# Performance work log

Hardware: AMD Instinct MI355X
Metric: run time of the kernel (lower is better)

The kernel has to match this reference:

```python
import jax, jax.numpy as jnp
import numpy as np

B, N, H = 4, 256, 512
P = 128  # game_physics_params


def _init(key, shape, scale=0.02):
    return jax.random.normal(key, shape, dtype=jnp.float32) * scale


def setup_inputs() -> dict:
    key = jax.random.key(0)
    ks = jax.random.split(key, 16)
    return {
        "object_features": jax.random.normal(ks[0], (B, N, H), dtype=jnp.float32),
        # physics_predictor: H -> 512 -> P
        "pp_w1": _init(ks[1], (H, 512)), "pp_b1": jnp.zeros((512,), jnp.float32),
        "pp_w2": _init(ks[2], (512, P)), "pp_b2": jnp.zeros((P,), jnp.float32),
        # collision_detector: 2H -> 256 -> 128 -> 1
        "cd_w1": _init(ks[3], (2 * H, 256)), "cd_b1": jnp.zeros((256,), jnp.float32),
        "cd_w2": _init(ks[4], (256, 128)), "cd_b2": jnp.zeros((128,), jnp.float32),
        "cd_w3": _init(ks[5], (128, 1)), "cd_b3": jnp.zeros((1,), jnp.float32),
        # velocity / force heads: H -> 3
        "vel_w": _init(ks[6], (H, 3)), "vel_b": jnp.zeros((3,), jnp.float32),
        "frc_w": _init(ks[7], (H, 3)), "frc_b": jnp.zeros((3,), jnp.float32),
    }


def reference(object_features, pp_w1, pp_b1, pp_w2, pp_b2,
              cd_w1, cd_b1, cd_w2, cd_b2, cd_w3, cd_b3,
              vel_w, vel_b, frc_w, frc_b):
    x = object_features  # [B, N, H]
    # physics predictor MLP
    p = jax.nn.relu(x @ pp_w1 + pp_b1) @ pp_w2 + pp_b2  # [B, N, P]
    mass = jax.nn.sigmoid(p[..., 0:1]) * 100.0
    friction = jax.nn.sigmoid(p[..., 1:2])
    elasticity = jax.nn.sigmoid(p[..., 2:3])
    density = jax.nn.sigmoid(p[..., 3:4]) * 10.0
    velocities = x @ vel_w + vel_b  # [B, N, 3]
    forces = x @ frc_w + frc_b      # [B, N, 3]

    # vectorized pairwise collision detection over upper-triangle pairs
    iu, ju = np.triu_indices(N, k=1)  # static index arrays, length Np = N(N-1)/2
    pairs = jnp.concatenate([x[:, iu], x[:, ju]], axis=-1)  # [B, Np, 2H]
    h = jax.nn.relu(pairs @ cd_w1 + cd_b1)
    h = jax.nn.relu(h @ cd_w2 + cd_b2)
    prob = jax.nn.sigmoid(h @ cd_w3 + cd_b3)[..., 0]  # [B, Np]
    collision_matrix = jnp.zeros((x.shape[0], N, N), dtype=x.dtype)
    collision_matrix = collision_matrix.at[:, iu, ju].set(prob).at[:, ju, iu].set(prob)

    return (mass, friction, elasticity, density, velocities, forces, collision_matrix)
```

## Files before the change

kernel.cpp:

```cpp
#include <hip/hip_runtime.h>
#include <hip/hip_bf16.h>

typedef __attribute__((ext_vector_type(8))) short bf16x8;
typedef __attribute__((ext_vector_type(4))) float f32x4;

__device__ __forceinline__ float sigmoidf_(float v) {
    return 1.0f / (1.0f + __expf(-v));
}
__device__ __forceinline__ short f2bf(float f) {
    union { __hip_bfloat16 h; short s; } cv;
    cv.h = __float2bfloat16(f);
    return cv.s;
}
__device__ __forceinline__ float bf2f(short s) {
    union { float f; unsigned u; } cv;
    cv.u = ((unsigned)(unsigned short)s) << 16;
    return cv.f;
}

__global__ __launch_bounds__(256) void convert_kernel(
    const float* __restrict__ x, const float* __restrict__ pp_w1,
    const float* __restrict__ cd_w1, const float* __restrict__ cd_w2,
    const float* __restrict__ pp_w2, const float* __restrict__ vel_w,
    const float* __restrict__ frc_w,
    __hip_bfloat16* __restrict__ xb, __hip_bfloat16* __restrict__ Wt,
    __hip_bfloat16* __restrict__ w2t, float* __restrict__ hw)
{
    __shared__ float ts[64][65];
    const int b = blockIdx.x, t = threadIdx.x;

    if (b < 256) {
        int base = b * 2048 + t * 8;
        float4 a = *(const float4*)(x + base);
        float4 c = *(const float4*)(x + base + 4);
        bf16x8 o;
        o[0] = f2bf(a.x); o[1] = f2bf(a.y); o[2] = f2bf(a.z); o[3] = f2bf(a.w);
        o[4] = f2bf(c.x); o[5] = f2bf(c.y); o[6] = f2bf(c.z); o[7] = f2bf(c.w);
        *(bf16x8*)(xb + base) = o;
        return;
    }
    if (b == 392) {
        for (int e = t; e < 5120; e += 256) {
            int h = e >> 9, k = e & 511;
            float v = (h < 4) ? pp_w2[k * 128 + h]
                    : (h < 7) ? vel_w[k * 3 + (h - 4)]
                              : frc_w[k * 3 + (h - 7)];
            hw[e] = v;
        }
        return;
    }

    const float* src; int ss, k0, n0, region;
    if (b < 320)      { int i = b - 256; src = pp_w1; ss = 512; k0 = (i >> 3) * 64; n0 = (i & 7) * 64; region = 0; }
    else if (b < 384) { int i = b - 320; src = cd_w1; ss = 256; k0 = (i >> 2) * 64; n0 = (i & 3) * 64; region = 1; }
    else              { int i = b - 384; src = cd_w2; ss = 128; k0 = (i >> 1) * 64; n0 = (i & 1) * 64; region = 2; }

    #pragma unroll
    for (int i = 0; i < 4; ++i) {
        int r = (t >> 4) + i * 16, c4 = (t & 15) * 4;
        *(float4*)&ts[r][c4] = *(const float4*)(src + (k0 + r) * ss + n0 + c4);
    }
    __syncthreads();
    #pragma unroll
    for (int i = 0; i < 4; ++i) {
        int nOut = (t >> 4) + i * 16, kc = (t & 15) * 4;
        ushort4 o;
        o.x = (unsigned short)f2bf(ts[kc + 0][nOut]);
        o.y = (unsigned short)f2bf(ts[kc + 1][nOut]);
        o.z = (unsigned short)f2bf(ts[kc + 2][nOut]);
        o.w = (unsigned short)f2bf(ts[kc + 3][nOut]);
        int gn = n0 + nOut, gk = k0 + kc;
        if (region == 0)      *(ushort4*)(Wt + gn * 512 + gk) = o;
        else if (region == 1) {
            int row = (gk < 512) ? (512 + gn) : (768 + gn);
            *(ushort4*)(Wt + row * 512 + (gk & 511)) = o;
        } else                *(ushort4*)(w2t + gn * 256 + gk) = o;
    }
}

__global__ __launch_bounds__(256) void gemm_kernel(
    const __hip_bfloat16* __restrict__ xb, const __hip_bfloat16* __restrict__ Wt,
    const float* __restrict__ pp_b1, const float* __restrict__ cd_b1,
    __hip_bfloat16* __restrict__ hidg, float* __restrict__ Ug,
    float* __restrict__ Vg)
{
    const int t = threadIdx.x;
    const int wave = t >> 6, lane = t & 63;
    const int l = lane & 15, q = lane >> 4;
    const int m0 = blockIdx.y * 32;
    const int n0 = blockIdx.x * 128 + wave * 32;

    const __hip_bfloat16* a0p = xb + (m0 + l) * 512 + q * 8;
    const __hip_bfloat16* a1p = a0p + 16 * 512;
    const __hip_bfloat16* b0p = Wt + (n0 + l) * 512 + q * 8;
    const __hip_bfloat16* b1p = b0p + 16 * 512;

    f32x4 acc00 = {}, acc01 = {}, acc10 = {}, acc11 = {};
    #pragma unroll
    for (int ks = 0; ks < 16; ++ks) {
        bf16x8 a0 = *(const bf16x8*)(a0p + ks * 32);
        bf16x8 a1 = *(const bf16x8*)(a1p + ks * 32);
        bf16x8 b0 = *(const bf16x8*)(b0p + ks * 32);
        bf16x8 b1 = *(const bf16x8*)(b1p + ks * 32);
        acc00 = __builtin_amdgcn_mfma_f32_16x16x32_bf16(a0, b0, acc00, 0, 0, 0);
        acc01 = __builtin_amdgcn_mfma_f32_16x16x32_bf16(a0, b1, acc01, 0, 0, 0);
        acc10 = __builtin_amdgcn_mfma_f32_16x16x32_bf16(a1, b0, acc10, 0, 0, 0);
        acc11 = __builtin_amdgcn_mfma_f32_16x16x32_bf16(a1, b1, acc11, 0, 0, 0);
    }

    const int c0 = n0 + l, c1 = n0 + 16 + l;
    #pragma unroll
    for (int mt = 0; mt < 2; ++mt) {
        const f32x4& A0 = mt ? acc10 : acc00;
        const f32x4& A1 = mt ? acc11 : acc01;
        if (n0 < 512) {
            float b0v = pp_b1[c0], b1v = pp_b1[c1];
            #pragma unroll
            for (int r = 0; r < 4; ++r) {
                int rg = m0 + mt * 16 + q * 4 + r;
                hidg[rg * 512 + c0] = __float2bfloat16(fmaxf(A0[r] + b0v, 0.f));
                hidg[rg * 512 + c1] = __float2bfloat16(fmaxf(A1[r] + b1v, 0.f));
            }
        } else if (n0 < 768) {
            float b0v = cd_b1[c0 - 512], b1v = cd_b1[c1 - 512];
            #pragma unroll
            for (int r = 0; r < 4; ++r) {
                int rg = m0 + mt * 16 + q * 4 + r;
                Ug[rg * 256 + (c0 - 512)] = A0[r] + b0v;
                Ug[rg * 256 + (c1 - 512)] = A1[r] + b1v;
            }
        } else {
            #pragma unroll
            for (int r = 0; r < 4; ++r) {
                int rg = m0 + mt * 16 + q * 4 + r;
                Vg[rg * 256 + (c0 - 768)] = A0[r];
                Vg[rg * 256 + (c1 - 768)] = A1[r];
            }
        }
    }
}

__global__ __launch_bounds__(256) void heads_kernel(
    const float* __restrict__ x, const __hip_bfloat16* __restrict__ hidg,
    const float* __restrict__ hw, const float* __restrict__ pp_b2,
    const float* __restrict__ vel_b, const float* __restrict__ frc_b,
    float* __restrict__ out)
{
    const int t = threadIdx.x, wave = t >> 6, lane = t & 63;
    const int row = blockIdx.x * 4 + wave;

    const float4* xr = (const float4*)(x + row * 512);
    float4 xa = xr[lane * 2], xc = xr[lane * 2 + 1];
    bf16x8 hb = *(const bf16x8*)(hidg + row * 512 + lane * 8);
    float hf[8];
    #pragma unroll
    for (int j = 0; j < 8; ++j) hf[j] = bf2f(hb[j]);

    #pragma unroll
    for (int h = 0; h < 10; ++h) {
        const float4* wr = (const float4*)(hw + h * 512);
        float4 wa = wr[lane * 2], wc = wr[lane * 2 + 1];
        float s;
        if (h < 4) {
            s = hf[0]*wa.x + hf[1]*wa.y + hf[2]*wa.z + hf[3]*wa.w
              + hf[4]*wc.x + hf[5]*wc.y + hf[6]*wc.z + hf[7]*wc.w;
        } else {
            s = xa.x*wa.x + xa.y*wa.y + xa.z*wa.z + xa.w*wa.w
              + xc.x*wc.x + xc.y*wc.y + xc.z*wc.z + xc.w*wc.w;
        }
        s += __shfl_xor(s, 1);  s += __shfl_xor(s, 2);
        s += __shfl_xor(s, 4);  s += __shfl_xor(s, 8);
        s += __shfl_xor(s, 16); s += __shfl_xor(s, 32);
        if (lane == 0) {
            if (h < 4) {
                float sg = sigmoidf_(s + pp_b2[h]);
                out[h * 1024 + row] = (h == 0) ? sg * 100.f : (h == 3) ? sg * 10.f : sg;
            } else if (h < 7) {
                out[4096 + row * 3 + (h - 4)] = s + vel_b[h - 4];
            } else {
                out[7168 + row * 3 + (h - 7)] = s + frc_b[h - 7];
            }
        }
    }
}

__global__ __launch_bounds__(512, 4) void pair_kernel(
    const float* __restrict__ Ug, const float* __restrict__ Vg,
    const __hip_bfloat16* __restrict__ w2t,
    const float* __restrict__ cd_b2, const float* __restrict__ cd_w3,
    const float* __restrict__ cd_b3, float* __restrict__ cm)
{
    __shared__ __align__(16) short w2s[32 * 128 * 8];

    const int tp = blockIdx.x;
    const int bz = blockIdx.y;
    int ti = 0;
    while ((ti + 1) * (65 - (ti + 1)) / 2 <= tp) ++ti;
    const int tj = ti + (tp - ti * (65 - ti) / 2);
    const int i0 = ti * 8, j0 = tj * 8;

    const int t = threadIdx.x;

    {
        #pragma unroll
        for (int it = 0; it < 8; ++it) {
            int e = it * 512 + t;
            int n = e >> 5, g = e & 31;
            uint4 d = *(const uint4*)(w2t + n * 256 + g * 8);
            *(uint4*)(w2s + (g * 128 + n) * 8) = d;
        }
    }
    __syncthreads();

    const int w = t >> 6, lane = t & 63;
    const int qd = w & 3;
    const int b = bz * 2 + (w >> 2);
    const int l = lane & 15, q = lane >> 4;

    const int pb = qd * 16 + l;
    const float* Up = Ug + (b * 256 + i0 + (pb >> 3)) * 256;
    const float* Vp = Vg + (b * 256 + j0 + (pb & 7)) * 256;

    f32x4 acc[8] = {};
    #pragma unroll
    for (int ks = 0; ks < 8; ++ks) {
        const int kk = ks * 32 + q * 8;
        float4 u0 = *(const float4*)(Up + kk);
        float4 u1 = *(const float4*)(Up + kk + 4);
        float4 v0 = *(const float4*)(Vp + kk);
        float4 v1 = *(const float4*)(Vp + kk + 4);
        bf16x8 afr;
        afr[0] = f2bf(fmaxf(u0.x + v0.x, 0.f));
        afr[1] = f2bf(fmaxf(u0.y + v0.y, 0.f));
        afr[2] = f2bf(fmaxf(u0.z + v0.z, 0.f));
        afr[3] = f2bf(fmaxf(u0.w + v0.w, 0.f));
        afr[4] = f2bf(fmaxf(u1.x + v1.x, 0.f));
        afr[5] = f2bf(fmaxf(u1.y + v1.y, 0.f));
        afr[6] = f2bf(fmaxf(u1.z + v1.z, 0.f));
        afr[7] = f2bf(fmaxf(u1.w + v1.w, 0.f));
        const short* wg = w2s + (ks * 4 + q) * 128 * 8;
        #pragma unroll
        for (int nt = 0; nt < 8; ++nt) {
            bf16x8 bfr = *(const bf16x8*)(wg + (nt * 16 + l) * 8);
            acc[nt] = __builtin_amdgcn_mfma_f32_16x16x32_bf16(afr, bfr, acc[nt], 0, 0, 0);
        }
    }

    float b2v[8], w3v[8];
    #pragma unroll
    for (int nt = 0; nt < 8; ++nt) {
        b2v[nt] = cd_b2[nt * 16 + l];
        w3v[nt] = cd_w3[nt * 16 + l];
    }
    const float b3 = cd_b3[0];
    float* base = cm + b * 65536;
    #pragma unroll
    for (int r = 0; r < 4; ++r) {
        float s = 0.f;
        #pragma unroll
        for (int nt = 0; nt < 8; ++nt)
            s += fmaxf(acc[nt][r] + b2v[nt], 0.f) * w3v[nt];
        s += __shfl_xor(s, 1);
        s += __shfl_xor(s, 2);
        s += __shfl_xor(s, 4);
        s += __shfl_xor(s, 8);
        if (l == 0) {
            const int p = qd * 16 + q * 4 + r;
            const int i = i0 + (p >> 3), j = j0 + (p & 7);
            float prob = sigmoidf_(s + b3);
            if (i < j) {
                base[i * 256 + j] = prob;
                base[j * 256 + i] = prob;
            } else if (i == j) {
                base[i * 256 + i] = 0.0f;
            }
        }
    }
}

extern "C" void kernel_launch(void* const* d_in, const int* in_sizes, int n_in,
                              void* d_out, int out_size, void* d_ws, size_t ws_size,
                              hipStream_t stream) {
    const float* x     = (const float*)d_in[0];
    const float* pp_w1 = (const float*)d_in[1];
    const float* pp_b1 = (const float*)d_in[2];
    const float* pp_w2 = (const float*)d_in[3];
    const float* pp_b2 = (const float*)d_in[4];
    const float* cd_w1 = (const float*)d_in[5];
    const float* cd_b1 = (const float*)d_in[6];
    const float* cd_w2 = (const float*)d_in[7];
    const float* cd_b2 = (const float*)d_in[8];
    const float* cd_w3 = (const float*)d_in[9];
    const float* cd_b3 = (const float*)d_in[10];
    const float* vel_w = (const float*)d_in[11];
    const float* vel_b = (const float*)d_in[12];
    const float* frc_w = (const float*)d_in[13];
    const float* frc_b = (const float*)d_in[14];

    float* out = (float*)d_out;
    float* Ug = (float*)d_ws;
    float* Vg = Ug + 262144;
    __hip_bfloat16* xb   = (__hip_bfloat16*)(Vg + 262144);
    __hip_bfloat16* Wt   = xb + 524288;
    __hip_bfloat16* hidg = Wt + 524288;
    __hip_bfloat16* w2t  = hidg + 524288;
    float* hw = (float*)(w2t + 32768);

    convert_kernel<<<dim3(393), dim3(256), 0, stream>>>(
        x, pp_w1, cd_w1, cd_w2, pp_w2, vel_w, frc_w, xb, Wt, w2t, hw);
    gemm_kernel<<<dim3(8, 32), dim3(256), 0, stream>>>(
        xb, Wt, pp_b1, cd_b1, hidg, Ug, Vg);
    heads_kernel<<<dim3(256), dim3(256), 0, stream>>>(
        x, hidg, hw, pp_b2, vel_b, frc_b, out);
    pair_kernel<<<dim3(528, 2), dim3(512), 0, stream>>>(
        Ug, Vg, w2t, cd_b2, cd_w3, cd_b3, out + 10240);
}
```

Baseline: 140.8 us.

## Fuse four kernels into one persistent kernel with grid-wide atomic barriers

Replaces the convert, GEMM, heads and pair kernels with a single 256-block persistent kernel. Phases are separated by software grid barriers built on atomic counters, which are reset by a memset before each launch. The pair stage now loops over work items in each block, with 4 waves per block instead of 8, and loads the w2 tile into shared memory once per block. This is meant to remove launch gaps between the kernels. In exchange the pair phase has lower parallelism, and correctness depends on all 256 blocks being resident at the same time.

```diff
diff --git a/kernel.cpp b/kernel.cpp
--- a/kernel.cpp
+++ b/kernel.cpp
@@ -18,28 +18,73 @@
     return cv.f;
 }
 
-__global__ __launch_bounds__(256) void convert_kernel(
-    const float* __restrict__ x, const float* __restrict__ pp_w1,
-    const float* __restrict__ cd_w1, const float* __restrict__ cd_w2,
-    const float* __restrict__ pp_w2, const float* __restrict__ vel_w,
-    const float* __restrict__ frc_w,
+__device__ __forceinline__ void gbar(unsigned* ctr) {
+    __syncthreads();
+    if (threadIdx.x == 0) {
+        __threadfence();
+        atomicAdd(ctr, 1u);
+        while (atomicAdd(ctr, 0u) < 256u) __builtin_amdgcn_s_sleep(1);
+        __threadfence();
+    }
+    __syncthreads();
+}
+
+__global__ __launch_bounds__(256, 2) void mega_kernel(
+    const float* __restrict__ x,
+    const float* __restrict__ pp_w1, const float* __restrict__ pp_b1,
+    const float* __restrict__ pp_w2, const float* __restrict__ pp_b2,
+    const float* __restrict__ cd_w1, const float* __restrict__ cd_b1,
+    const float* __restrict__ cd_w2, const float* __restrict__ cd_b2,
+    const float* __restrict__ cd_w3, const float* __restrict__ cd_b3,
+    const float* __restrict__ vel_w, const float* __restrict__ vel_b,
+    const float* __restrict__ frc_w, const float* __restrict__ frc_b,
+    float* __restrict__ out, float* __restrict__ Ug, float* __restrict__ Vg,
     __hip_bfloat16* __restrict__ xb, __hip_bfloat16* __restrict__ Wt,
-    __hip_bfloat16* __restrict__ w2t, float* __restrict__ hw)
+    __hip_bfloat16* __restrict__ hidg, __hip_bfloat16* __restrict__ w2t,
+    float* __restrict__ hw, unsigned* __restrict__ bar)
 {
-    __shared__ float ts[64][65];
-    const int b = blockIdx.x, t = threadIdx.x;
-
-    if (b < 256) {
-        int base = b * 2048 + t * 8;
+    __shared__ __align__(16) char smem[65536];
+    const int blk = blockIdx.x, t = threadIdx.x;
+    const int wave = t >> 6, lane = t & 63;
+    const int l = lane & 15, q = lane >> 4;
+
+    {
+        int base = blk * 2048 + t * 8;
         float4 a = *(const float4*)(x + base);
         float4 c = *(const float4*)(x + base + 4);
         bf16x8 o;
         o[0] = f2bf(a.x); o[1] = f2bf(a.y); o[2] = f2bf(a.z); o[3] = f2bf(a.w);
         o[4] = f2bf(c.x); o[5] = f2bf(c.y); o[6] = f2bf(c.z); o[7] = f2bf(c.w);
         *(bf16x8*)(xb + base) = o;
-        return;
-    }
-    if (b == 392) {
+    }
+    if (blk < 136) {
+        float (*ts)[65] = (float(*)[65])smem;
+        const float* src; int ss, k0, n0, region;
+        if (blk < 64)       { src = pp_w1; ss = 512; k0 = (blk >> 3) * 64; n0 = (blk & 7) * 64; region = 0; }
+        else if (blk < 128) { int i = blk - 64;  src = cd_w1; ss = 256; k0 = (i >> 2) * 64; n0 = (i & 3) * 64; region = 1; }
+        else                { int i = blk - 128; src = cd_w2; ss = 128; k0 = (i >> 1) * 64; n0 = (i & 1) * 64; region = 2; }
+        #pragma unroll
+        for (int i = 0; i < 4; ++i) {
+            int r = (t >> 4) + i * 16, c4 = (t & 15) * 4;
+            *(float4*)&ts[r][c4] = *(const float4*)(src + (k0 + r) * ss + n0 + c4);
+        }
+        __syncthreads();
+        #pragma unroll
+        for (int i = 0; i < 4; ++i) {
+            int nOut = (t >> 4) + i * 16, kc = (t & 15) * 4;
+            ushort4 o;
+            o.x = (unsigned short)f2bf(ts[kc + 0][nOut]);
+            o.y = (unsigned short)f2bf(ts[kc + 1][nOut]);
+            o.z = (unsigned short)f2bf(ts[kc + 2][nOut]);
+            o.w = (unsigned short)f2bf(ts[kc + 3][nOut]);
+            int gn = n0 + nOut, gk = k0 + kc;
+            if (region == 0)      *(ushort4*)(Wt + gn * 512 + gk) = o;
+            else if (region == 1) {
+                int row = (gk < 512) ? (512 + gn) : (768 + gn);
+                *(ushort4*)(Wt + row * 512 + (gk & 511)) = o;
+            } else                *(ushort4*)(w2t + gn * 256 + gk) = o;
+        }
+    } else if (blk == 136) {
         for (int e = t; e < 5120; e += 256) {
             int h = e >> 9, k = e & 511;
             float v = (h < 4) ? pp_w2[k * 128 + h]
@@ -47,232 +92,175 @@
                               : frc_w[k * 3 + (h - 7)];
             hw[e] = v;
         }
-        return;
-    }
-
-    const float* src; int ss, k0, n0, region;
-    if (b < 320)      { int i = b - 256; src = pp_w1; ss = 512; k0 = (i >> 3) * 64; n0 = (i & 7) * 64; region = 0; }
-    else if (b < 384) { int i = b - 320; src = cd_w1; ss = 256; k0 = (i >> 2) * 64; n0 = (i & 3) * 64; region = 1; }
-    else              { int i = b - 384; src = cd_w2; ss = 128; k0 = (i >> 1) * 64; n0 = (i & 1) * 64; region = 2; }
-
-    #pragma unroll
-    for (int i = 0; i < 4; ++i) {
-        int r = (t >> 4) + i * 16, c4 = (t & 15) * 4;
-        *(float4*)&ts[r][c4] = *(const float4*)(src + (k0 + r) * ss + n0 + c4);
-    }
-    __syncthreads();
-    #pragma unroll
-    for (int i = 0; i < 4; ++i) {
-        int nOut = (t >> 4) + i * 16, kc = (t & 15) * 4;
-        ushort4 o;
-        o.x = (unsigned short)f2bf(ts[kc + 0][nOut]);
-        o.y = (unsigned short)f2bf(ts[kc + 1][nOut]);
-        o.z = (unsigned short)f2bf(ts[kc + 2][nOut]);
-        o.w = (unsigned short)f2bf(ts[kc + 3][nOut]);
-        int gn = n0 + nOut, gk = k0 + kc;
-        if (region == 0)      *(ushort4*)(Wt + gn * 512 + gk) = o;
-        else if (region == 1) {
-            int row = (gk < 512) ? (512 + gn) : (768 + gn);
-            *(ushort4*)(Wt + row * 512 + (gk & 511)) = o;
-        } else                *(ushort4*)(w2t + gn * 256 + gk) = o;
-    }
-}
-
-__global__ __launch_bounds__(256) void gemm_kernel(
-    const __hip_bfloat16* __restrict__ xb, const __hip_bfloat16* __restrict__ Wt,
-    const float* __restrict__ pp_b1, const float* __restrict__ cd_b1,
-    __hip_bfloat16* __restrict__ hidg, float* __restrict__ Ug,
-    float* __restrict__ Vg)
-{
-    const int t = threadIdx.x;
-    const int wave = t >> 6, lane = t & 63;
-    const int l = lane & 15, q = lane >> 4;
-    const int m0 = blockIdx.y * 32;
-    const int n0 = blockIdx.x * 128 + wave * 32;
-
-    const __hip_bfloat16* a0p = xb + (m0 + l) * 512 + q * 8;
-    const __hip_bfloat16* a1p = a0p + 16 * 512;
-    const __hip_bfloat16* b0p = Wt + (n0 + l) * 512 + q * 8;
-    const __hip_bfloat16* b1p = b0p + 16 * 512;
-
-    f32x4 acc00 = {}, acc01 = {}, acc10 = {}, acc11 = {};
-    #pragma unroll
-    for (int ks = 0; ks < 16; ++ks) {
-        bf16x8 a0 = *(const bf16x8*)(a0p + ks * 32);
-        bf16x8 a1 = *(const bf16x8*)(a1p + ks * 32);
-        bf16x8 b0 = *(const bf16x8*)(b0p + ks * 32);
-        bf16x8 b1 = *(const bf16x8*)(b1p + ks * 32);
-        acc00 = __builtin_amdgcn_mfma_f32_16x16x32_bf16(a0, b0, acc00, 0, 0, 0);
-        acc01 = __builtin_amdgcn_mfma_f32_16x16x32_bf16(a0, b1, acc01, 0, 0, 0);
-        acc10 = __builtin_amdgcn_mfma_f32_16x16x32_bf16(a1, b0, acc10, 0, 0, 0);
-        acc11 = __builtin_amdgcn_mfma_f32_16x16x32_bf16(a1, b1, acc11, 0, 0, 0);
-    }
-
-    const int c0 = n0 + l, c1 = n0 + 16 + l;
-    #pragma unroll
-    for (int mt = 0; mt < 2; ++mt) {
-        const f32x4& A0 = mt ? acc10 : acc00;
-        const f32x4& A1 = mt ? acc11 : acc01;
-        if (n0 < 512) {
-            float b0v = pp_b1[c0], b1v = pp_b1[c1];
-            #pragma unroll
-            for (int r = 0; r < 4; ++r) {
-                int rg = m0 + mt * 16 + q * 4 + r;
-                hidg[rg * 512 + c0] = __float2bfloat16(fmaxf(A0[r] + b0v, 0.f));
-                hidg[rg * 512 + c1] = __float2bfloat16(fmaxf(A1[r] + b1v, 0.f));
-            }
-        } else if (n0 < 768) {
-            float b0v = cd_b1[c0 - 512], b1v = cd_b1[c1 - 512];
-            #pragma unroll
-            for (int r = 0; r < 4; ++r) {
-                int rg = m0 + mt * 16 + q * 4 + r;
-                Ug[rg * 256 + (c0 - 512)] = A0[r] + b0v;
-                Ug[rg * 256 + (c1 - 512)] = A1[r] + b1v;
-            }
-        } else {
-            #pragma unroll
-            for (int r = 0; r < 4; ++r) {
-                int rg = m0 + mt * 16 + q * 4 + r;
-                Vg[rg * 256 + (c0 - 768)] = A0[r];
-                Vg[rg * 256 + (c1 - 768)] = A1[r];
-            }
-        }
-    }
-}
-
-__global__ __launch_bounds__(256) void heads_kernel(
-    const float* __restrict__ x, const __hip_bfloat16* __restrict__ hidg,
-    const float* __restrict__ hw, const float* __restrict__ pp_b2,
-    const float* __restrict__ vel_b, const float* __restrict__ frc_b,
-    float* __restrict__ out)
-{
-    const int t = threadIdx.x, wave = t >> 6, lane = t & 63;
-    const int row = blockIdx.x * 4 + wave;
-
-    const float4* xr = (const float4*)(x + row * 512);
-    float4 xa = xr[lane * 2], xc = xr[lane * 2 + 1];
-    bf16x8 hb = *(const bf16x8*)(hidg + row * 512 + lane * 8);
-    float hf[8];
-    #pragma unroll
-    for (int j = 0; j < 8; ++j) hf[j] = bf2f(hb[j]);
-
-    #pragma unroll
-    for (int h = 0; h < 10; ++h) {
-        const float4* wr = (const float4*)(hw + h * 512);
-        float4 wa = wr[lane * 2], wc = wr[lane * 2 + 1];
-        float s;
-        if (h < 4) {
-            s = hf[0]*wa.x + hf[1]*wa.y + hf[2]*wa.z + hf[3]*wa.w
-              + hf[4]*wc.x + hf[5]*wc.y + hf[6]*wc.z + hf[7]*wc.w;
-        } else {
-            s = xa.x*wa.x + xa.y*wa.y + xa.z*wa.z + xa.w*wa.w
-              + xc.x*wc.x + xc.y*wc.y + xc.z*wc.z + xc.w*wc.w;
-        }
-        s += __shfl_xor(s, 1);  s += __shfl_xor(s, 2);
-        s += __shfl_xor(s, 4);  s += __shfl_xor(s, 8);
-        s += __shfl_xor(s, 16); s += __shfl_xor(s, 32);
-        if (lane == 0) {
-            if (h < 4) {
-                float sg = sigmoidf_(s + pp_b2[h]);
-                out[h * 1024 + row] = (h == 0) ? sg * 100.f : (h == 3) ? sg * 10.f : sg;
-            } else if (h < 7) {
-                out[4096 + row * 3 + (h - 4)] = s + vel_b[h - 4];
-            } else {
-                out[7168 + row * 3 + (h - 7)] = s + frc_b[h - 7];
-            }
-        }
-    }
-}
-
-__global__ __launch_bounds__(512, 4) void pair_kernel(
-    const float* __restrict__ Ug, const float* __restrict__ Vg,
-    const __hip_bfloat16* __restrict__ w2t,
-    const float* __restrict__ cd_b2, const float* __restrict__ cd_w3,
-    const float* __restrict__ cd_b3, float* __restrict__ cm)
-{
-    __shared__ __align__(16) short w2s[32 * 128 * 8];
-
-    const int tp = blockIdx.x;
-    const int bz = blockIdx.y;
-    int ti = 0;
-    while ((ti + 1) * (65 - (ti + 1)) / 2 <= tp) ++ti;
-    const int tj = ti + (tp - ti * (65 - ti) / 2);
-    const int i0 = ti * 8, j0 = tj * 8;
-
-    const int t = threadIdx.x;
-
-    {
-        #pragma unroll
-        for (int it = 0; it < 8; ++it) {
-            int e = it * 512 + t;
+    }
+    gbar(bar + 0);
+
+    {
+        short* w2s = (short*)smem;
+        #pragma unroll
+        for (int it = 0; it < 16; ++it) {
+            int e = it * 256 + t;
             int n = e >> 5, g = e & 31;
             uint4 d = *(const uint4*)(w2t + n * 256 + g * 8);
             *(uint4*)(w2s + (g * 128 + n) * 8) = d;
         }
     }
-    __syncthreads();
-
-    const int w = t >> 6, lane = t & 63;
-    const int qd = w & 3;
-    const int b = bz * 2 + (w >> 2);
-    const int l = lane & 15, q = lane >> 4;
-
-    const int pb = qd * 16 + l;
-    const float* Up = Ug + (b * 256 + i0 + (pb >> 3)) * 256;
-    const float* Vp = Vg + (b * 256 + j0 + (pb & 7)) * 256;
-
-    f32x4 acc[8] = {};
-    #pragma unroll
-    for (int ks = 0; ks < 8; ++ks) {
-        const int kk = ks * 32 + q * 8;
-        float4 u0 = *(const float4*)(Up + kk);
-        float4 u1 = *(const float4*)(Up + kk + 4);
-        float4 v0 = *(const float4*)(Vp + kk);
-        float4 v1 = *(const float4*)(Vp + kk + 4);
-        bf16x8 afr;
-        afr[0] = f2bf(fmaxf(u0.x + v0.x, 0.f));
-        afr[1] = f2bf(fmaxf(u0.y + v0.y, 0.f));
-        afr[2] = f2bf(fmaxf(u0.z + v0.z, 0.f));
-        afr[3] = f2bf(fmaxf(u0.w + v0.w, 0.f));
-        afr[4] = f2bf(fmaxf(u1.x + v1.x, 0.f));
-        afr[5] = f2bf(fmaxf(u1.y + v1.y, 0.f));
-        afr[6] = f2bf(fmaxf(u1.z + v1.z, 0.f));
-        afr[7] = f2bf(fmaxf(u1.w + v1.w, 0.f));
-        const short* wg = w2s + (ks * 4 + q) * 128 * 8;
+
+    {
+        const int m0 = (blk >> 3) * 32;
+        const int n0 = (blk & 7) * 128 + wave * 32;
+        const __hip_bfloat16* a0p = xb + (m0 + l) * 512 + q * 8;
+        const __hip_bfloat16* a1p = a0p + 16 * 512;
+        const __hip_bfloat16* b0p = Wt + (n0 + l) * 512 + q * 8;
+        const __hip_bfloat16* b1p = b0p + 16 * 512;
+        f32x4 acc00 = {}, acc01 = {}, acc10 = {}, acc11 = {};
+        #pragma unroll
+        for (int ks = 0; ks < 16; ++ks) {
+            bf16x8 a0 = *(const bf16x8*)(a0p + ks * 32);
+            bf16x8 a1 = *(const bf16x8*)(a1p + ks * 32);
+            bf16x8 b0 = *(const bf16x8*)(b0p + ks * 32);
+            bf16x8 b1 = *(const bf16x8*)(b1p + ks * 32);
+            acc00 = __builtin_amdgcn_mfma_f32_16x16x32_bf16(a0, b0, acc00, 0, 0, 0);
+            acc01 = __builtin_amdgcn_mfma_f32_16x16x32_bf16(a0, b1, acc01, 0, 0, 0);
+            acc10 = __builtin_amdgcn_mfma_f32_16x16x32_bf16(a1, b0, acc10, 0, 0, 0);
+            acc11 = __builtin_amdgcn_mfma_f32_16x16x32_bf16(a1, b1, acc11, 0, 0, 0);
+        }
+        const int c0 = n0 + l, c1 = n0 + 16 + l;
+        #pragma unroll
+        for (int mt = 0; mt < 2; ++mt) {
+            const f32x4& A0 = mt ? acc10 : acc00;
+            const f32x4& A1 = mt ? acc11 : acc01;
+            if (n0 < 512) {
+                float b0v = pp_b1[c0], b1v = pp_b1[c1];
+                #pragma unroll
+                for (int r = 0; r < 4; ++r) {
+                    int rg = m0 + mt * 16 + q * 4 + r;
+                    hidg[rg * 512 + c0] = __float2bfloat16(fmaxf(A0[r] + b0v, 0.f));
+                    hidg[rg * 512 + c1] = __float2bfloat16(fmaxf(A1[r] + b1v, 0.f));
+                }
+            } else if (n0 < 768) {
+                float b0v = cd_b1[c0 - 512], b1v = cd_b1[c1 - 512];
+                #pragma unroll
+                for (int r = 0; r < 4; ++r) {
+                    int rg = m0 + mt * 16 + q * 4 + r;
+                    Ug[rg * 256 + (c0 - 512)] = A0[r] + b0v;
+                    Ug[rg * 256 + (c1 - 512)] = A1[r] + b1v;
+                }
+            } else {
+                #pragma unroll
+                for (int r = 0; r < 4; ++r) {
+                    int rg = m0 + mt * 16 + q * 4 + r;
+                    Vg[rg * 256 + (c0 - 768)] = A0[r];
+                    Vg[rg * 256 + (c1 - 768)] = A1[r];
+                }
+            }
+        }
+    }
+    gbar(bar + 1);
+
+    {
+        const int row = blk * 4 + wave;
+        const float4* xr = (const float4*)(x + row * 512);
+        float4 xa = xr[lane * 2], xc = xr[lane * 2 + 1];
+        bf16x8 hb = *(const bf16x8*)(hidg + row * 512 + lane * 8);
+        float hf[8];
+        #pragma unroll
+        for (int j = 0; j < 8; ++j) hf[j] = bf2f(hb[j]);
+        #pragma unroll
+        for (int h = 0; h < 10; ++h) {
+            const float4* wr = (const float4*)(hw + h * 512);
+            float4 wa = wr[lane * 2], wc = wr[lane * 2 + 1];
+            float s;
+            if (h < 4) {
+                s = hf[0]*wa.x + hf[1]*wa.y + hf[2]*wa.z + hf[3]*wa.w
+                  + hf[4]*wc.x + hf[5]*wc.y + hf[6]*wc.z + hf[7]*wc.w;
+            } else {
+                s = xa.x*wa.x + xa.y*wa.y + xa.z*wa.z + xa.w*wa.w
+                  + xc.x*wc.x + xc.y*wc.y + xc.z*wc.z + xc.w*wc.w;
+            }
+            s += __shfl_xor(s, 1);  s += __shfl_xor(s, 2);
+            s += __shfl_xor(s, 4);  s += __shfl_xor(s, 8);
+            s += __shfl_xor(s, 16); s += __shfl_xor(s, 32);
+            if (lane == 0) {
+                if (h < 4) {
+                    float sg = sigmoidf_(s + pp_b2[h]);
+                    out[h * 1024 + row] = (h == 0) ? sg * 100.f : (h == 3) ? sg * 10.f : sg;
+                } else if (h < 7) {
+                    out[4096 + row * 3 + (h - 4)] = s + vel_b[h - 4];
+                } else {
+                    out[7168 + row * 3 + (h - 7)] = s + frc_b[h - 7];
+                }
+            }
+        }
+    }
+
+    {
+        const short* w2s = (const short*)smem;
+        float b2v[8], w3v[8];
         #pragma unroll
         for (int nt = 0; nt < 8; ++nt) {
-            bf16x8 bfr = *(const bf16x8*)(wg + (nt * 16 + l) * 8);
-            acc[nt] = __builtin_amdgcn_mfma_f32_16x16x32_bf16(afr, bfr, acc[nt], 0, 0, 0);
-        }
-    }
-
-    float b2v[8], w3v[8];
-    #pragma unroll
-    for (int nt = 0; nt < 8; ++nt) {
-        b2v[nt] = cd_b2[nt * 16 + l];
-        w3v[nt] = cd_w3[nt * 16 + l];
-    }
-    const float b3 = cd_b3[0];
-    float* base = cm + b * 65536;
-    #pragma unroll
-    for (int r = 0; r < 4; ++r) {
-        float s = 0.f;
-        #pragma unroll
-        for (int nt = 0; nt < 8; ++nt)
-            s += fmaxf(acc[nt][r] + b2v[nt], 0.f) * w3v[nt];
-        s += __shfl_xor(s, 1);
-        s += __shfl_xor(s, 2);
-        s += __shfl_xor(s, 4);
-        s += __shfl_xor(s, 8);
-        if (l == 0) {
-            const int p = qd * 16 + q * 4 + r;
-            const int i = i0 + (p >> 3), j = j0 + (p & 7);
-            float prob = sigmoidf_(s + b3);
-            if (i < j) {
-                base[i * 256 + j] = prob;
-                base[j * 256 + i] = prob;
-            } else if (i == j) {
-                base[i * 256 + i] = 0.0f;
+            b2v[nt] = cd_b2[nt * 16 + l];
+            w3v[nt] = cd_w3[nt * 16 + l];
+        }
+        const float b3 = cd_b3[0];
+        for (int item = blk; item < 2112; item += 256) {
+            const int tp = item >> 2, b = item & 3;
+            int ti = 0;
+            while ((ti + 1) * (65 - (ti + 1)) / 2 <= tp) ++ti;
+            const int tj = ti + (tp - ti * (65 - ti) / 2);
+            const int i0 = ti * 8, j0 = tj * 8;
+
+            const int pb = wave * 16 + l;
+            const float* Up = Ug + (b * 256 + i0 + (pb >> 3)) * 256;
+            const float* Vp = Vg + (b * 256 + j0 + (pb & 7)) * 256;
+
+            f32x4 acc[8] = {};
+            #pragma unroll
+            for (int ks = 0; ks < 8; ++ks) {
+                const int kk = ks * 32 + q * 8;
+                float4 u0 = *(const float4*)(Up + kk);
+                float4 u1 = *(const float4*)(Up + kk + 4);
+                float4 v0 = *(const float4*)(Vp + kk);
+                float4 v1 = *(const float4*)(Vp + kk + 4);
+                bf16x8 afr;
+                afr[0] = f2bf(fmaxf(u0.x + v0.x, 0.f));
+                afr[1] = f2bf(fmaxf(u0.y + v0.y, 0.f));
+                afr[2] = f2bf(fmaxf(u0.z + v0.z, 0.f));
+                afr[3] = f2bf(fmaxf(u0.w + v0.w, 0.f));
+                afr[4] = f2bf(fmaxf(u1.x + v1.x, 0.f));
+                afr[5] = f2bf(fmaxf(u1.y + v1.y, 0.f));
+                afr[6] = f2bf(fmaxf(u1.z + v1.z, 0.f));
+                afr[7] = f2bf(fmaxf(u1.w + v1.w, 0.f));
+                const short* wg = w2s + (ks * 4 + q) * 1024;
+                #pragma unroll
+                for (int nt = 0; nt < 8; ++nt) {
+                    bf16x8 bfr = *(const bf16x8*)(wg + (nt * 16 + l) * 8);
+                    acc[nt] = __builtin_amdgcn_mfma_f32_16x16x32_bf16(afr, bfr, acc[nt], 0, 0, 0);
+                }
+            }
+
+            float* base = out + 10240 + b * 65536;
+            #pragma unroll
+            for (int r = 0; r < 4; ++r) {
+                float s = 0.f;
+                #pragma unroll
+                for (int nt = 0; nt < 8; ++nt)
+                    s += fmaxf(acc[nt][r] + b2v[nt], 0.f) * w3v[nt];
+                s += __shfl_xor(s, 1);
+                s += __shfl_xor(s, 2);
+                s += __shfl_xor(s, 4);
+                s += __shfl_xor(s, 8);
+                if (l == 0) {
+                    const int p = wave * 16 + q * 4 + r;
+                    const int i = i0 + (p >> 3), j = j0 + (p & 7);
+                    float prob = sigmoidf_(s + b3);
+                    if (i < j) {
+                        base[i * 256 + j] = prob;
+                        base[j * 256 + i] = prob;
+                    } else if (i == j) {
+                        base[i * 256 + i] = 0.0f;
+                    }
+                }
             }
         }
     }
@@ -305,13 +293,11 @@
     __hip_bfloat16* hidg = Wt + 524288;
     __hip_bfloat16* w2t  = hidg + 524288;
     float* hw = (float*)(w2t + 32768);
-
-    convert_kernel<<<dim3(393), dim3(256), 0, stream>>>(
-        x, pp_w1, cd_w1, cd_w2, pp_w2, vel_w, frc_w, xb, Wt, w2t, hw);
-    gemm_kernel<<<dim3(8, 32), dim3(256), 0, stream>>>(
-        xb, Wt, pp_b1, cd_b1, hidg, Ug, Vg);
-    heads_kernel<<<dim3(256), dim3(256), 0, stream>>>(
-        x, hidg, hw, pp_b2, vel_b, frc_b, out);
-    pair_kernel<<<dim3(528, 2), dim3(512), 0, stream>>>(
-        Ug, Vg, w2t, cd_b2, cd_w3, cd_b3, out + 10240);
-}
+    unsigned* bar = (unsigned*)((char*)d_ws + (8u << 20));
+
+    hipMemsetAsync(bar, 0, 256, stream);
+    mega_kernel<<<dim3(256), dim3(256), 0, stream>>>(
+        x, pp_w1, pp_b1, pp_w2, pp_b2, cd_w1, cd_b1, cd_w2, cd_b2,
+        cd_w3, cd_b3, vel_w, vel_b, frc_w, frc_b,
+        out, Ug, Vg, xb, Wt, hidg, w2t, hw, bar);
+}
```

New measurement: 217.9 us. 54.8% more time.

## Fuse heads into pair kernel and read W2 from global instead of LDS

Applied to the files above, without the earlier changes.

The heads computation and the pairwise collision MLP are merged into one tail kernel launch, with extra blocks (bx >= 528) doing the per-row heads work. This removes one kernel launch and its tail gap. The pair path drops the LDS staging of cd_w2 and the __syncthreads, and instead loads B fragments directly from global/L2. Each wave now computes two 16-pair M tiles that share each B fragment, and blocks shrink to 256 threads with launch bounds 256,3. The risk is more global/L2 traffic for the weights and higher register pressure from the doubled accumulators.

```diff
diff --git a/kernel.cpp b/kernel.cpp
--- a/kernel.cpp
+++ b/kernel.cpp
@@ -140,109 +140,104 @@
     }
 }
 
-__global__ __launch_bounds__(256) void heads_kernel(
+__global__ __launch_bounds__(256, 3) void tail_kernel(
     const float* __restrict__ x, const __hip_bfloat16* __restrict__ hidg,
     const float* __restrict__ hw, const float* __restrict__ pp_b2,
     const float* __restrict__ vel_b, const float* __restrict__ frc_b,
-    float* __restrict__ out)
-{
-    const int t = threadIdx.x, wave = t >> 6, lane = t & 63;
-    const int row = blockIdx.x * 4 + wave;
-
-    const float4* xr = (const float4*)(x + row * 512);
-    float4 xa = xr[lane * 2], xc = xr[lane * 2 + 1];
-    bf16x8 hb = *(const bf16x8*)(hidg + row * 512 + lane * 8);
-    float hf[8];
-    #pragma unroll
-    for (int j = 0; j < 8; ++j) hf[j] = bf2f(hb[j]);
-
-    #pragma unroll
-    for (int h = 0; h < 10; ++h) {
-        const float4* wr = (const float4*)(hw + h * 512);
-        float4 wa = wr[lane * 2], wc = wr[lane * 2 + 1];
-        float s;
-        if (h < 4) {
-            s = hf[0]*wa.x + hf[1]*wa.y + hf[2]*wa.z + hf[3]*wa.w
-              + hf[4]*wc.x + hf[5]*wc.y + hf[6]*wc.z + hf[7]*wc.w;
-        } else {
-            s = xa.x*wa.x + xa.y*wa.y + xa.z*wa.z + xa.w*wa.w
-              + xc.x*wc.x + xc.y*wc.y + xc.z*wc.z + xc.w*wc.w;
-        }
-        s += __shfl_xor(s, 1);  s += __shfl_xor(s, 2);
-        s += __shfl_xor(s, 4);  s += __shfl_xor(s, 8);
-        s += __shfl_xor(s, 16); s += __shfl_xor(s, 32);
-        if (lane == 0) {
-            if (h < 4) {
-                float sg = sigmoidf_(s + pp_b2[h]);
-                out[h * 1024 + row] = (h == 0) ? sg * 100.f : (h == 3) ? sg * 10.f : sg;
-            } else if (h < 7) {
-                out[4096 + row * 3 + (h - 4)] = s + vel_b[h - 4];
-            } else {
-                out[7168 + row * 3 + (h - 7)] = s + frc_b[h - 7];
-            }
-        }
-    }
-}
-
-__global__ __launch_bounds__(512, 4) void pair_kernel(
     const float* __restrict__ Ug, const float* __restrict__ Vg,
     const __hip_bfloat16* __restrict__ w2t,
     const float* __restrict__ cd_b2, const float* __restrict__ cd_w3,
-    const float* __restrict__ cd_b3, float* __restrict__ cm)
+    const float* __restrict__ cd_b3, float* __restrict__ out)
 {
-    __shared__ __align__(16) short w2s[32 * 128 * 8];
-
-    const int tp = blockIdx.x;
-    const int bz = blockIdx.y;
+    const int bx = blockIdx.x, bz = blockIdx.y, t = threadIdx.x;
+    const int w = t >> 6, lane = t & 63;
+    const int l = lane & 15, q = lane >> 4;
+
+    if (bx >= 528) {
+        const int idx = (bx - 528) + 128 * bz;
+        const int row = idx * 4 + w;
+        const float4* xr = (const float4*)(x + row * 512);
+        float4 xa = xr[lane * 2], xc = xr[lane * 2 + 1];
+        bf16x8 hb = *(const bf16x8*)(hidg + row * 512 + lane * 8);
+        float hf[8];
+        #pragma unroll
+        for (int j = 0; j < 8; ++j) hf[j] = bf2f(hb[j]);
+        #pragma unroll
+        for (int h = 0; h < 10; ++h) {
+            const float4* wr = (const float4*)(hw + h * 512);
+            float4 wa = wr[lane * 2], wc = wr[lane * 2 + 1];
+            float s;
+            if (h < 4) {
+                s = hf[0]*wa.x + hf[1]*wa.y + hf[2]*wa.z + hf[3]*wa.w
+                  + hf[4]*wc.x + hf[5]*wc.y + hf[6]*wc.z + hf[7]*wc.w;
+            } else {
+                s = xa.x*wa.x + xa.y*wa.y + xa.z*wa.z + xa.w*wa.w
+                  + xc.x*wc.x + xc.y*wc.y + xc.z*wc.z + xc.w*wc.w;
+            }
+            s += __shfl_xor(s, 1);  s += __shfl_xor(s, 2);
+            s += __shfl_xor(s, 4);  s += __shfl_xor(s, 8);
+            s += __shfl_xor(s, 16); s += __shfl_xor(s, 32);
+            if (lane == 0) {
+                if (h < 4) {
+                    float sg = sigmoidf_(s + pp_b2[h]);
+                    out[h * 1024 + row] = (h == 0) ? sg * 100.f : (h == 3) ? sg * 10.f : sg;
+                } else if (h < 7) {
+                    out[4096 + row * 3 + (h - 4)] = s + vel_b[h - 4];
+                } else {
+                    out[7168 + row * 3 + (h - 7)] = s + frc_b[h - 7];
+                }
+            }
+        }
+        return;
+    }
+
+    const int tp = bx;
     int ti = 0;
     while ((ti + 1) * (65 - (ti + 1)) / 2 <= tp) ++ti;
     const int tj = ti + (tp - ti * (65 - ti) / 2);
     const int i0 = ti * 8, j0 = tj * 8;
 
-    const int t = threadIdx.x;
-
-    {
-        #pragma unroll
-        for (int it = 0; it < 8; ++it) {
-            int e = it * 512 + t;
-            int n = e >> 5, g = e & 31;
-            uint4 d = *(const uint4*)(w2t + n * 256 + g * 8);
-            *(uint4*)(w2s + (g * 128 + n) * 8) = d;
-        }
-    }
-    __syncthreads();
-
-    const int w = t >> 6, lane = t & 63;
-    const int qd = w & 3;
-    const int b = bz * 2 + (w >> 2);
-    const int l = lane & 15, q = lane >> 4;
-
-    const int pb = qd * 16 + l;
-    const float* Up = Ug + (b * 256 + i0 + (pb >> 3)) * 256;
-    const float* Vp = Vg + (b * 256 + j0 + (pb & 7)) * 256;
-
-    f32x4 acc[8] = {};
+    const int b = bz * 2 + (w >> 1);
+    const int s0 = (w & 1) * 32;
+
+    const int pA = s0 + l, pB = pA + 16;
+    const float* UA = Ug + (b * 256 + i0 + (pA >> 3)) * 256;
+    const float* VA = Vg + (b * 256 + j0 + (pA & 7)) * 256;
+    const float* UB = Ug + (b * 256 + i0 + (pB >> 3)) * 256;
+    const float* VB = Vg + (b * 256 + j0 + (pB & 7)) * 256;
+    const __hip_bfloat16* wB = w2t + l * 256 + q * 8;
+
+    f32x4 acc0[8] = {}, acc1[8] = {};
     #pragma unroll
     for (int ks = 0; ks < 8; ++ks) {
         const int kk = ks * 32 + q * 8;
-        float4 u0 = *(const float4*)(Up + kk);
-        float4 u1 = *(const float4*)(Up + kk + 4);
-        float4 v0 = *(const float4*)(Vp + kk);
-        float4 v1 = *(const float4*)(Vp + kk + 4);
-        bf16x8 afr;
-        afr[0] = f2bf(fmaxf(u0.x + v0.x, 0.f));
-        afr[1] = f2bf(fmaxf(u0.y + v0.y, 0.f));
-        afr[2] = f2bf(fmaxf(u0.z + v0.z, 0.f));
-        afr[3] = f2bf(fmaxf(u0.w + v0.w, 0.f));
-        afr[4] = f2bf(fmaxf(u1.x + v1.x, 0.f));
-        afr[5] = f2bf(fmaxf(u1.y + v1.y, 0.f));
-        afr[6] = f2bf(fmaxf(u1.z + v1.z, 0.f));
-        afr[7] = f2bf(fmaxf(u1.w + v1.w, 0.f));
-        const short* wg = w2s + (ks * 4 + q) * 128 * 8;
+        float4 ua0 = *(const float4*)(UA + kk), ua1 = *(const float4*)(UA + kk + 4);
+        float4 va0 = *(const float4*)(VA + kk), va1 = *(const float4*)(VA + kk + 4);
+        bf16x8 afrA;
+        afrA[0] = f2bf(fmaxf(ua0.x + va0.x, 0.f));
+        afrA[1] = f2bf(fmaxf(ua0.y + va0.y, 0.f));
+        afrA[2] = f2bf(fmaxf(ua0.z + va0.z, 0.f));
+        afrA[3] = f2bf(fmaxf(ua0.w + va0.w, 0.f));
+        afrA[4] = f2bf(fmaxf(ua1.x + va1.x, 0.f));
+        afrA[5] = f2bf(fmaxf(ua1.y + va1.y, 0.f));
+        afrA[6] = f2bf(fmaxf(ua1.z + va1.z, 0.f));
+        afrA[7] = f2bf(fmaxf(ua1.w + va1.w, 0.f));
+        float4 ub0 = *(const float4*)(UB + kk), ub1 = *(const float4*)(UB + kk + 4);
+        float4 vb0 = *(const float4*)(VB + kk), vb1 = *(const float4*)(VB + kk + 4);
+        bf16x8 afrB;
+        afrB[0] = f2bf(fmaxf(ub0.x + vb0.x, 0.f));
+        afrB[1] = f2bf(fmaxf(ub0.y + vb0.y, 0.f));
+        afrB[2] = f2bf(fmaxf(ub0.z + vb0.z, 0.f));
+        afrB[3] = f2bf(fmaxf(ub0.w + vb0.w, 0.f));
+        afrB[4] = f2bf(fmaxf(ub1.x + vb1.x, 0.f));
+        afrB[5] = f2bf(fmaxf(ub1.y + vb1.y, 0.f));
+        afrB[6] = f2bf(fmaxf(ub1.z + vb1.z, 0.f));
+        afrB[7] = f2bf(fmaxf(ub1.w + vb1.w, 0.f));
         #pragma unroll
         for (int nt = 0; nt < 8; ++nt) {
-            bf16x8 bfr = *(const bf16x8*)(wg + (nt * 16 + l) * 8);
-            acc[nt] = __builtin_amdgcn_mfma_f32_16x16x32_bf16(afr, bfr, acc[nt], 0, 0, 0);
+            bf16x8 bfr = *(const bf16x8*)(wB + nt * 4096 + ks * 32);
+            acc0[nt] = __builtin_amdgcn_mfma_f32_16x16x32_bf16(afrA, bfr, acc0[nt], 0, 0, 0);
+            acc1[nt] = __builtin_amdgcn_mfma_f32_16x16x32_bf16(afrB, bfr, acc1[nt], 0, 0, 0);
         }
     }
 
@@ -253,26 +248,31 @@
         w3v[nt] = cd_w3[nt * 16 + l];
     }
     const float b3 = cd_b3[0];
-    float* base = cm + b * 65536;
-    #pragma unroll
-    for (int r = 0; r < 4; ++r) {
-        float s = 0.f;
+    float* base = out + 10240 + b * 65536;
+    #pragma unroll
+    for (int mt = 0; mt < 2; ++mt) {
         #pragma unroll
-        for (int nt = 0; nt < 8; ++nt)
-            s += fmaxf(acc[nt][r] + b2v[nt], 0.f) * w3v[nt];
-        s += __shfl_xor(s, 1);
-        s += __shfl_xor(s, 2);
-        s += __shfl_xor(s, 4);
-        s += __shfl_xor(s, 8);
-        if (l == 0) {
-            const int p = qd * 16 + q * 4 + r;
-            const int i = i0 + (p >> 3), j = j0 + (p & 7);
-            float prob = sigmoidf_(s + b3);
-            if (i < j) {
-                base[i * 256 + j] = prob;
-                base[j * 256 + i] = prob;
-            } else if (i == j) {
-                base[i * 256 + i] = 0.0f;
+        for (int r = 0; r < 4; ++r) {
+            float s = 0.f;
+            #pragma unroll
+            for (int nt = 0; nt < 8; ++nt) {
+                const f32x4& a = mt ? acc1[nt] : acc0[nt];
+                s += fmaxf(a[r] + b2v[nt], 0.f) * w3v[nt];
+            }
+            s += __shfl_xor(s, 1);
+            s += __shfl_xor(s, 2);
+            s += __shfl_xor(s, 4);
+            s += __shfl_xor(s, 8);
+            if (l == 0) {
+                const int p = s0 + mt * 16 + q * 4 + r;
+                const int i = i0 + (p >> 3), j = j0 + (p & 7);
+                float prob = sigmoidf_(s + b3);
+                if (i < j) {
+                    base[i * 256 + j] = prob;
+                    base[j * 256 + i] = prob;
+                } else if (i == j) {
+                    base[i * 256 + i] = 0.0f;
+                }
             }
         }
     }
@@ -310,8 +310,7 @@
         x, pp_w1, cd_w1, cd_w2, pp_w2, vel_w, frc_w, xb, Wt, w2t, hw);
     gemm_kernel<<<dim3(8, 32), dim3(256), 0, stream>>>(
         xb, Wt, pp_b1, cd_b1, hidg, Ug, Vg);
-    heads_kernel<<<dim3(256), dim3(256), 0, stream>>>(
-        x, hidg, hw, pp_b2, vel_b, frc_b, out);
-    pair_kernel<<<dim3(528, 2), dim3(512), 0, stream>>>(
-        Ug, Vg, w2t, cd_b2, cd_w3, cd_b3, out + 10240);
-}
+    tail_kernel<<<dim3(656, 2), dim3(256), 0, stream>>>(
+        x, hidg, hw, pp_b2, vel_b, frc_b,
+        Ug, Vg, w2t, cd_b2, cd_w3, cd_b3, out);
+}
```

New measurement: 154.1 us. 1.09x slower.
